# Kernel optimization log

Measured on AMD Instinct MI355X. Metric: run time of the kernel, lower is better.

Reference implementation:

```python
import jax, jax.numpy as jnp
import numpy as np

D_IN = 4097   # 4096 obj feat + 1 depth
D_H1 = 512
D_H2 = 256
N_HEADS = 4
D_HEAD = D_H2 // N_HEADS
D_FF = 512


def setup_inputs() -> dict:
    key = jax.random.key(0)
    ks = jax.random.split(key, 20)
    B, T, N = 2, 100, 30
    s = lambda *sh: 1.0 / np.sqrt(sh[0])
    inp = {
        "object_features": jax.random.normal(ks[0], (B, T, N, 4096), jnp.float32),
        "object_depths": jax.random.uniform(ks[1], (B, T, N, 1), jnp.float32),
        # spatial encoder (2-layer fully-connected message passing)
        "W1a": jax.random.normal(ks[2], (D_IN, D_H1), jnp.float32) * s(D_IN),
        "W2a": jax.random.normal(ks[3], (D_IN, D_H1), jnp.float32) * s(D_IN),
        "b1a": jnp.zeros((D_H1,), jnp.float32),
        "W1b": jax.random.normal(ks[4], (D_H1, D_H2), jnp.float32) * s(D_H1),
        "W2b": jax.random.normal(ks[5], (D_H1, D_H2), jnp.float32) * s(D_H1),
        "b1b": jnp.zeros((D_H2,), jnp.float32),
        # temporal transformer encoder layer (post-LN)
        "Wq": jax.random.normal(ks[6], (D_H2, D_H2), jnp.float32) * s(D_H2),
        "Wk": jax.random.normal(ks[7], (D_H2, D_H2), jnp.float32) * s(D_H2),
        "Wv": jax.random.normal(ks[8], (D_H2, D_H2), jnp.float32) * s(D_H2),
        "Wo": jax.random.normal(ks[9], (D_H2, D_H2), jnp.float32) * s(D_H2),
        "ln1_g": jnp.ones((D_H2,), jnp.float32),
        "ln1_b": jnp.zeros((D_H2,), jnp.float32),
        "Wf1": jax.random.normal(ks[10], (D_H2, D_FF), jnp.float32) * s(D_H2),
        "bf1": jnp.zeros((D_FF,), jnp.float32),
        "Wf2": jax.random.normal(ks[11], (D_FF, D_H2), jnp.float32) * s(D_FF),
        "bf2": jnp.zeros((D_H2,), jnp.float32),
        "ln2_g": jnp.ones((D_H2,), jnp.float32),
        "ln2_b": jnp.zeros((D_H2,), jnp.float32),
        # classifier
        "Wc": jax.random.normal(ks[12], (D_H2, 1), jnp.float32) * s(D_H2),
        "bc": jnp.zeros((1,), jnp.float32),
    }
    return inp


def _layer_norm(x, g, b, eps=1e-5):
    mu = jnp.mean(x, axis=-1, keepdims=True)
    var = jnp.var(x, axis=-1, keepdims=True)
    return (x - mu) * jax.lax.rsqrt(var + eps) * g + b


def _forward(object_features, object_depths, W1a, W2a, b1a, W1b, W2b, b1b,
             Wq, Wk, Wv, Wo, ln1_g, ln1_b, Wf1, bf1, Wf2, bf2, ln2_g, ln2_b,
             Wc, bc):
    B, T, N, _ = object_features.shape
    x = jnp.concatenate([object_features, object_depths], axis=-1)  # (B,T,N,4097)
    # fully-connected graph (torch.combinations, both directions):
    # aggregated message for node i = mean over all j != i.
    def mp(h, Ws, Wn, b):
        neigh = (jnp.sum(h, axis=2, keepdims=True) - h) / (N - 1)
        return jax.nn.relu(h @ Ws + neigh @ Wn + b)
    h = mp(x, W1a, W2a, b1a)      # (B,T,N,512)
    h = mp(h, W1b, W2b, b1b)      # (B,T,N,256)
    g = jnp.mean(h, axis=2)       # global mean pool -> (B,T,256)
    # temporal transformer encoder (self-attention over T, post-LN)
    q = (g @ Wq).reshape(B, T, N_HEADS, D_HEAD)
    k = (g @ Wk).reshape(B, T, N_HEADS, D_HEAD)
    v = (g @ Wv).reshape(B, T, N_HEADS, D_HEAD)
    scores = jnp.einsum("bthd,bshd->bhts", q, k) / np.sqrt(D_HEAD)
    attn = jax.nn.softmax(scores, axis=-1)
    ctx = jnp.einsum("bhts,bshd->bthd", attn, v).reshape(B, T, D_H2) @ Wo
    y = _layer_norm(g + ctx, ln1_g, ln1_b)
    ff = jax.nn.relu(y @ Wf1 + bf1) @ Wf2 + bf2
    z = _layer_norm(y + ff, ln2_g, ln2_b)  # (B,T,256)
    # dropout is identity in eval mode -> probs2 == probs, uncertainty == 0
    logits = (z @ Wc + bc).squeeze(-1)     # (B,T)
    probs = jax.nn.sigmoid(logits)
    uncertainty = jnp.zeros_like(probs)
    return probs, uncertainty


def reference(object_features, object_depths, W1a, W2a, b1a, W1b, W2b, b1b,
              Wq, Wk, Wv, Wo, ln1_g, ln1_b, Wf1, bf1, Wf2, bf2, ln2_g, ln2_b,
              Wc, bc):
    return _forward(object_features, object_depths, W1a, W2a, b1a, W1b, W2b,
                    b1b, Wq, Wk, Wv, Wo, ln1_g, ln1_b, Wf1, bf1, Wf2, bf2,
                    ln2_g, ln2_b, Wc, bc)
```

## Files before the change

kernel.cpp:

```cpp
#include <hip/hip_runtime.h>
#include <hip/hip_bf16.h>
#include <stdint.h>

typedef unsigned short u16;
typedef __attribute__((ext_vector_type(8))) short short8;
typedef __attribute__((ext_vector_type(4))) float floatx4;
typedef __attribute__((ext_vector_type(4))) unsigned short ushort4_t;

#define BT 200
#define NOBJ 30
#define KP2 4224
#define DIN 4097
#define DH1 512
#define DH2 256
#define DFF 512
#define MPAD 6016
#define CHZ 176
#define NBIGW (132*16)
#define NSMALL 512
#define NCONV (BT*3)
#define NZERO 128

__device__ __forceinline__ u16 f2bf(float f) {
    union { float f; uint32_t u; } c; c.f = f;
    uint32_t u = c.u;
    u += 0x7FFF + ((u >> 16) & 1);
    return (u16)(u >> 16);
}

__device__ __forceinline__ void load16_lds(const u16* g, u16* l) {
    __builtin_amdgcn_global_load_lds(
        (const __attribute__((address_space(1))) void*)g,
        (__attribute__((address_space(3))) void*)l, 16, 0, 0);
}

__device__ __forceinline__ size_t tile_off(int ytile, int row, int c8) {
    int z = c8 / CHZ, rem = c8 - z * CHZ;
    int i = rem >> 3, kw = rem & 7;
    int ks = kw ^ (row & 7);
    return ((((size_t)(ytile * 3 + z) * 22 + i) * 128 + row) * 64) + ks * 8;
}

__global__ void prep_all(const float* __restrict__ W1a, const float* __restrict__ W2a,
                         const float* __restrict__ W1b, const float* __restrict__ W2b,
                         const float* __restrict__ feat, const float* __restrict__ depth,
                         u16* __restrict__ Wc1T, u16* __restrict__ W2aTs,
                         u16* __restrict__ Wc2T, u16* __restrict__ W2bTs,
                         u16* __restrict__ XbT, u16* __restrict__ SbT,
                         float* __restrict__ zeroBase, size_t zeroQuads) {
    __shared__ float t1[32][33];
    __shared__ float t2[32][33];
    int bid = blockIdx.x, tid = threadIdx.x;
    if (bid < NCONV) {
        int bt = bid / 3;
        int c8 = (bid % 3) * 256 + tid;
        if (c8 >= 528) return;
        int k8 = c8 * 8;
        int zc = c8 / CHZ, rem = c8 - zc * CHZ;
        int ic = rem >> 3, kwc = rem & 7;
        float s[8] = {};
        if (k8 < 4096) {
            const float* fb = feat + (size_t)bt * NOBJ * 4096 + k8;
            #pragma unroll 1
            for (int n0 = 0; n0 < NOBJ; n0 += 6) {
                float4 va[6], vb[6];
                #pragma unroll
                for (int u = 0; u < 6; u++) {
                    const float* p = fb + (size_t)(n0 + u) * 4096;
                    va[u] = *(const float4*)p;
                    vb[u] = *(const float4*)(p + 4);
                }
                #pragma unroll
                for (int u = 0; u < 6; u++) {
                    int r = bt * NOBJ + n0 + u;
                    float v[8] = {va[u].x, va[u].y, va[u].z, va[u].w,
                                  vb[u].x, vb[u].y, vb[u].z, vb[u].w};
                    short8 o;
                    #pragma unroll
                    for (int e = 0; e < 8; e++) { s[e] += v[e]; o[e] = (short)f2bf(v[e]); }
                    size_t off = ((((size_t)((r >> 7) * 3 + zc) * 22 + ic) * 128
                                   + (r & 127)) * 64) + (size_t)(kwc ^ (r & 7)) * 8;
                    *(short8*)(XbT + off) = o;
                }
            }
        } else {
            for (int n = 0; n < NOBJ; n++) {
                int r = bt * NOBJ + n;
                short8 o = {};
                if (k8 == 4096) {
                    float d = depth[r];
                    s[0] += d;
                    o[0] = (short)f2bf(d);
                }
                size_t off = ((((size_t)((r >> 7) * 3 + zc) * 22 + ic) * 128
                               + (r & 127)) * 64) + (size_t)(kwc ^ (r & 7)) * 8;
                *(short8*)(XbT + off) = o;
            }
        }
        short8 so;
        #pragma unroll
        for (int e = 0; e < 8; e++) so[e] = (short)f2bf(s[e]);
        {
            int r = bt;
            size_t off = ((((size_t)((r >> 7) * 3 + zc) * 22 + ic) * 128
                           + (r & 127)) * 64) + (size_t)(kwc ^ (r & 7)) * 8;
            *(short8*)(SbT + off) = so;
        }
    } else if (bid < NCONV + NZERO) {
        int zid = bid - NCONV;
        float4* p = (float4*)zeroBase;
        float4 zz = {0.f, 0.f, 0.f, 0.f};
        for (size_t idx = (size_t)zid * 256 + tid; idx < zeroQuads; idx += (size_t)NZERO * 256)
            p[idx] = zz;
    } else if (bid < NCONV + NZERO + NSMALL) {
        int idx = (bid - NCONV - NZERO) * 256 + tid;
        int j = idx >> 9, k = idx & 511;
        float a = W1b[k * DH2 + j];
        float b = W2b[k * DH2 + j] * (1.f / 29.f);
        Wc2T[j * DH1 + k]  = f2bf(a - b);
        W2bTs[j * DH1 + k] = f2bf(b);
    } else {
        int b2 = bid - NCONV - NZERO - NSMALL;
        int kb = (b2 % 132) * 32, jb = (b2 / 132) * 32;
        int tx = tid & 31, ty = tid >> 5;
        #pragma unroll
        for (int r = 0; r < 32; r += 8) {
            int k = kb + ty + r, j = jb + tx;
            float a = 0.f, b = 0.f;
            if (k < DIN) { a = W1a[k * DH1 + j]; b = W2a[k * DH1 + j]; }
            float bs = b * (1.f / 29.f);
            t1[ty + r][tx] = a - bs;
            t2[ty + r][tx] = bs;
        }
        __syncthreads();
        #pragma unroll
        for (int r = 0; r < 32; r += 8) {
            int j = jb + ty + r, k = kb + tx;
            int x = j >> 7, row = j & 127;
            size_t off = tile_off(x, row, k >> 3) + (k & 7);
            Wc1T[off]  = f2bf(t1[tx][ty + r]);
            W2aTs[off] = f2bf(t2[tx][ty + r]);
        }
    }
}

__global__ __launch_bounds__(256) void gemmA(
    const u16* __restrict__ XbT, const u16* __restrict__ WaT,
    const u16* __restrict__ SbT, const u16* __restrict__ WsT,
    float* __restrict__ hacc, float* __restrict__ uOut) {
    __shared__ __align__(16) u16 Al[8192];
    __shared__ __align__(16) u16 Bl[8192];
    int bid = blockIdx.x;
    const u16 *Abase, *Bbase;
    float* outF;
    int m0, n0, M;
    if (bid < 564) {
        int x = bid & 3, y = (bid >> 2) % 47, z = bid / 188;
        Abase = XbT + (size_t)((y * 3 + z) * 22) * 8192;
        Bbase = WaT + (size_t)((x * 3 + z) * 22) * 8192;
        outF = hacc; M = 6000; m0 = y * 128; n0 = x * 128;
    } else {
        int rem = bid - 564;
        int x = rem & 3, y = (rem >> 2) & 1, z = rem >> 3;
        Abase = SbT + (size_t)((y * 3 + z) * 22) * 8192;
        Bbase = WsT + (size_t)((x * 3 + z) * 22) * 8192;
        outF = uOut; M = BT; m0 = y * 128; n0 = x * 128;
    }
    int tid = threadIdx.x, lane = tid & 63, w = tid >> 6;
    floatx4 acc[4][4] = {};
    int lrow = lane & 15, q = lane >> 4;
    int wm = (w & 1) * 64, wn = (w >> 1) * 64;
    int swz = lrow & 7;

    for (int i = 0; i < 22; i++) {
        const u16* as = Abase + (size_t)i * 8192;
        const u16* bs = Bbase + (size_t)i * 8192;
        #pragma unroll
        for (int it = 0; it < 4; it++) {
            load16_lds(as + (it * 256 + tid) * 8, Al + it * 2048 + w * 512);
            load16_lds(bs + (it * 256 + tid) * 8, Bl + it * 2048 + w * 512);
        }
        __syncthreads();
        #pragma unroll
        for (int h = 0; h < 2; h++) {
            int ci = h * 4 + q;
            int so = (ci ^ swz) * 8;
            short8 af[4], bfv[4];
            #pragma unroll
            for (int ii = 0; ii < 4; ii++)
                af[ii] = *(short8*)(Al + (wm + ii * 16 + lrow) * 64 + so);
            #pragma unroll
            for (int j = 0; j < 4; j++)
                bfv[j] = *(short8*)(Bl + (wn + j * 16 + lrow) * 64 + so);
            #pragma unroll
            for (int ii = 0; ii < 4; ii++)
                #pragma unroll
                for (int j = 0; j < 4; j++)
                    acc[ii][j] = __builtin_amdgcn_mfma_f32_16x16x32_bf16(af[ii], bfv[j], acc[ii][j], 0, 0, 0);
        }
        __syncthreads();
    }

    #pragma unroll
    for (int ii = 0; ii < 4; ii++)
        #pragma unroll
        for (int j = 0; j < 4; j++)
            #pragma unroll
            for (int r = 0; r < 4; r++) {
                int row = m0 + wm + ii * 16 + q * 4 + r;
                int col = n0 + wn + j * 16 + lrow;
                if (row < M)
                    atomicAdd(&outF[(size_t)row * DH1 + col], acc[ii][j][r]);
            }
}

__global__ __launch_bounds__(256) void gemmB(
    const u16* __restrict__ hb, const u16* __restrict__ Wc2T,
    const u16* __restrict__ Shb, const u16* __restrict__ W2bTs,
    float* __restrict__ hacc2, float* __restrict__ u2Out) {
    __shared__ __align__(16) u16 Al[64 * 64];
    __shared__ __align__(16) u16 Bl[128 * 64];
    int bid = blockIdx.x;
    const u16 *A, *B;
    float* outF;
    int m0, n0, kbeg, M;
    if (bid < 376) {
        int x = bid & 1, y = (bid >> 1) % 94, z = bid / 188;
        A = hb; B = Wc2T; outF = hacc2; M = 6000;
        m0 = y * 64; n0 = x * 128; kbeg = z * 256;
    } else {
        int rem = bid - 376;
        int x = rem & 1, y = (rem >> 1) & 3, z = rem >> 3;
        A = Shb; B = W2bTs; outF = u2Out; M = BT;
        m0 = y * 64; n0 = x * 128; kbeg = z * 256;
    }
    int kend = kbeg + 256;
    const int N = DH2, K = DH1;
    int tid = threadIdx.x;
    int lane = tid & 63, w = tid >> 6;
    int srow = tid >> 3, kslot = tid & 7;
    floatx4 acc[2][4] = {};
    int lrow = lane & 15, q = lane >> 4;
    int wm = (w & 1) * 32, wn = (w >> 1) * 64;
    int swz = lrow & 7;

    for (int kb = kbeg; kb < kend; kb += 64) {
        #pragma unroll
        for (int it = 0; it < 2; it++) {
            int row = it * 32 + srow;
            int kph = kslot ^ (row & 7);
            load16_lds(A + (size_t)(m0 + row) * K + kb + kph * 8,
                       Al + it * 2048 + w * 512);
        }
        #pragma unroll
        for (int it = 0; it < 4; it++) {
            int row = it * 32 + srow;
            int kph = kslot ^ (row & 7);
            load16_lds(B + (size_t)(n0 + row) * K + kb + kph * 8,
                       Bl + it * 2048 + w * 512);
        }
        __syncthreads();
        #pragma unroll
        for (int h = 0; h < 2; h++) {
            int ci = h * 4 + q;
            int so = (ci ^ swz) * 8;
            short8 af[2], bfv[4];
            #pragma unroll
            for (int i = 0; i < 2; i++)
                af[i] = *(short8*)(Al + (wm + i * 16 + lrow) * 64 + so);
            #pragma unroll
            for (int j = 0; j < 4; j++)
                bfv[j] = *(short8*)(Bl + (wn + j * 16 + lrow) * 64 + so);
            #pragma unroll
            for (int i = 0; i < 2; i++)
                #pragma unroll
                for (int j = 0; j < 4; j++)
                    acc[i][j] = __builtin_amdgcn_mfma_f32_16x16x32_bf16(af[i], bfv[j], acc[i][j], 0, 0, 0);
        }
        __syncthreads();
    }

    #pragma unroll
    for (int i = 0; i < 2; i++)
        #pragma unroll
        for (int j = 0; j < 4; j++)
            #pragma unroll
            for (int r = 0; r < 4; r++) {
                int row = m0 + wm + i * 16 + q * 4 + r;
                int col = n0 + wn + j * 16 + lrow;
                if (row < M)
                    atomicAdd(&outF[(size_t)row * N + col], acc[i][j][r]);
            }
}

__global__ void reduce1(const float* __restrict__ hacc, const float* __restrict__ u,
                        const float* __restrict__ b1a,
                        u16* __restrict__ hb, u16* __restrict__ Shb) {
    __shared__ float sl[128];
    int bt = blockIdx.x, c0 = blockIdx.y * 128;
    int lc = threadIdx.x & 127, rp = threadIdx.x >> 7;
    int col = c0 + lc;
    float ub = u[bt * DH1 + col] + b1a[col];
    float s = 0.f;
    for (int n = rp; n < NOBJ; n += 2) {
        float v = hacc[(size_t)(bt * NOBJ + n) * DH1 + col] + ub;
        v = v > 0.f ? v : 0.f;
        hb[(size_t)(bt * NOBJ + n) * DH1 + col] = f2bf(v);
        s += v;
    }
    if (rp == 0) sl[lc] = s;
    __syncthreads();
    if (rp == 1) Shb[bt * DH1 + col] = f2bf(sl[lc] + s);
}

__global__ void reduce2_qkv(const float* __restrict__ hacc2, const float* __restrict__ u2,
                            const float* __restrict__ b1b,
                            const float* __restrict__ Wq, const float* __restrict__ Wk,
                            const float* __restrict__ Wv,
                            float* __restrict__ g, float* __restrict__ q,
                            float* __restrict__ k, float* __restrict__ v) {
    __shared__ float gl[DH2];
    int bt = blockIdx.x, j = threadIdx.x;
    float ub = u2[bt * DH2 + j] + b1b[j];
    float a = 0.f;
    for (int n = 0; n < NOBJ; n++) {
        float vv = hacc2[(size_t)(bt * NOBJ + n) * DH2 + j] + ub;
        a += vv > 0.f ? vv : 0.f;
    }
    a *= (1.f / 30.f);
    gl[j] = a;
    g[bt * DH2 + j] = a;
    __syncthreads();
    float aq = 0.f, ak = 0.f, av = 0.f;
    for (int kk = 0; kk < DH2; kk++) {
        float x = gl[kk];
        aq += x * Wq[kk * DH2 + j];
        ak += x * Wk[kk * DH2 + j];
        av += x * Wv[kk * DH2 + j];
    }
    q[bt * DH2 + j] = aq;
    k[bt * DH2 + j] = ak;
    v[bt * DH2 + j] = av;
}

__device__ __forceinline__ float block_sum256(float v, volatile float* red) {
    #pragma unroll
    for (int o = 32; o > 0; o >>= 1) v += __shfl_down(v, o);
    int w = threadIdx.x >> 6;
    __syncthreads();
    if ((threadIdx.x & 63) == 0) red[w] = v;
    __syncthreads();
    return red[0] + red[1] + red[2] + red[3];
}

__global__ void attn_head(const float* __restrict__ qg, const float* __restrict__ kg,
                          const float* __restrict__ vg, const float* __restrict__ g,
                          const float* __restrict__ Wo,
                          const float* __restrict__ ln1g, const float* __restrict__ ln1b,
                          const float* __restrict__ Wf1, const float* __restrict__ bf1,
                          const float* __restrict__ Wf2, const float* __restrict__ bf2,
                          const float* __restrict__ ln2g, const float* __restrict__ ln2b,
                          const float* __restrict__ Wc, const float* __restrict__ bc,
                          float* __restrict__ out) {
    __shared__ float ql[DH2];
    __shared__ float scl[4][128];
    __shared__ float ctxl[DH2];
    __shared__ float yl[DH2];
    __shared__ float ffl[DFF];
    __shared__ float red[4];
    int row = blockIdx.x, tid = threadIdx.x;
    int base = (row >= 100) ? 100 : 0;
    ql[tid] = qg[row * DH2 + tid];
    __syncthreads();

    for (int p = tid; p < 512; p += 256) {
        int h = p >> 7, s = p & 127;
        if (s < 100) {
            const float* kr = kg + (size_t)(base + s) * DH2 + h * 64;
            float a = 0.f;
            #pragma unroll 8
            for (int d = 0; d < 64; d++) a += ql[h * 64 + d] * kr[d];
            scl[h][s] = a * 0.125f;
        }
    }
    __syncthreads();

    {
        int w = tid >> 6, lane = tid & 63;
        int s2 = 64 + lane;
        float a  = scl[w][lane];
        float b2 = (s2 < 100) ? scl[w][s2] : -1e30f;
        float m = fmaxf(a, b2);
        #pragma unroll
        for (int o = 32; o > 0; o >>= 1) m = fmaxf(m, __shfl_down(m, o));
        m = __shfl(m, 0);
        float e1 = __expf(a - m);
        float e2 = (s2 < 100) ? __expf(b2 - m) : 0.f;
        float sm = e1 + e2;
        #pragma unroll
        for (int o = 32; o > 0; o >>= 1) sm += __shfl_down(sm, o);
        sm = __shfl(sm, 0);
        float r = 1.f / sm;
        scl[w][lane] = e1 * r;
        if (s2 < 100) scl[w][s2] = e2 * r;
    }
    __syncthreads();

    {
        int h = tid >> 6;
        float o = 0.f;
        for (int s = 0; s < 100; s++)
            o += scl[h][s] * vg[(size_t)(base + s) * DH2 + tid];
        ctxl[tid] = o;
    }
    __syncthreads();

    float o = 0.f;
    for (int kk = 0; kk < DH2; kk++) o += ctxl[kk] * Wo[kk * DH2 + tid];
    float t = g[row * DH2 + tid] + o;
    float mu  = block_sum256(t, red) * (1.f / DH2);
    float ex2 = block_sum256(t * t, red) * (1.f / DH2);
    float y = (t - mu) * rsqrtf(ex2 - mu * mu + 1e-5f) * ln1g[tid] + ln1b[tid];
    yl[tid] = y;
    __syncthreads();
    for (int jj = tid; jj < DFF; jj += 256) {
        float a = bf1[jj];
        for (int kk = 0; kk < DH2; kk++) a += yl[kk] * Wf1[kk * DFF + jj];
        ffl[jj] = a > 0.f ? a : 0.f;
    }
    __syncthreads();
    float o2 = bf2[tid];
    for (int kk = 0; kk < DFF; kk++) o2 += ffl[kk] * Wf2[kk * DH2 + tid];
    float z0 = y + o2;
    float mu2  = block_sum256(z0, red) * (1.f / DH2);
    float ex22 = block_sum256(z0 * z0, red) * (1.f / DH2);
    float z = (z0 - mu2) * rsqrtf(ex22 - mu2 * mu2 + 1e-5f) * ln2g[tid] + ln2b[tid];
    float logit = block_sum256(z * Wc[tid], red) + bc[0];
    if (tid == 0) {
        out[row]      = 1.f / (1.f + __expf(-logit));
        out[BT + row] = 0.f;
    }
}

extern "C" void kernel_launch(void* const* d_in, const int* in_sizes, int n_in,
                              void* d_out, int out_size, void* d_ws, size_t ws_size,
                              hipStream_t stream) {
    const float* feat  = (const float*)d_in[0];
    const float* depth = (const float*)d_in[1];
    const float* W1a = (const float*)d_in[2];
    const float* W2a = (const float*)d_in[3];
    const float* b1a = (const float*)d_in[4];
    const float* W1b = (const float*)d_in[5];
    const float* W2b = (const float*)d_in[6];
    const float* b1b = (const float*)d_in[7];
    const float* Wq  = (const float*)d_in[8];
    const float* Wk  = (const float*)d_in[9];
    const float* Wv  = (const float*)d_in[10];
    const float* Wo  = (const float*)d_in[11];
    const float* ln1g = (const float*)d_in[12];
    const float* ln1b = (const float*)d_in[13];
    const float* Wf1 = (const float*)d_in[14];
    const float* bf1 = (const float*)d_in[15];
    const float* Wf2 = (const float*)d_in[16];
    const float* bf2 = (const float*)d_in[17];
    const float* ln2g = (const float*)d_in[18];
    const float* ln2b = (const float*)d_in[19];
    const float* Wc  = (const float*)d_in[20];
    const float* bc  = (const float*)d_in[21];
    float* out = (float*)d_out;
    char* ws = (char*)d_ws;

    size_t off = 0;
    u16* XbT   = (u16*)(ws + off); off += (size_t)MPAD * KP2 * 2;
    u16* SbT   = (u16*)(ws + off); off += (size_t)256 * KP2 * 2;
    u16* Wc1T  = (u16*)(ws + off); off += (size_t)DH1 * KP2 * 2;
    u16* W2aTs = (u16*)(ws + off); off += (size_t)DH1 * KP2 * 2;
    u16* Wc2T  = (u16*)(ws + off); off += (size_t)DH2 * DH1 * 2;
    u16* W2bTs = (u16*)(ws + off); off += (size_t)DH2 * DH1 * 2;
    u16* Shb   = (u16*)(ws + off); off += (size_t)256 * DH1 * 2;
    char* zBase = ws + off;
    float* hacc  = (float*)(ws + off); off += (size_t)6000 * DH1 * 4;
    float* hacc2 = (float*)(ws + off); off += (size_t)6000 * DH2 * 4;
    float* u     = (float*)(ws + off); off += (size_t)BT * DH1 * 4;
    float* u2    = (float*)(ws + off); off += (size_t)BT * DH2 * 4;
    size_t zeroQuads = (size_t)(ws + off - zBase) / 16;
    u16* hb = XbT;
    float* g = (float*)SbT;
    float* q = g + BT * DH2;
    float* k = q + BT * DH2;
    float* v = k + BT * DH2;

    prep_all<<<NBIGW + NSMALL + NCONV + NZERO, 256, 0, stream>>>(
        W1a, W2a, W1b, W2b, feat, depth,
        Wc1T, W2aTs, Wc2T, W2bTs, XbT, SbT, (float*)zBase, zeroQuads);
    gemmA<<<564 + 24, 256, 0, stream>>>(XbT, Wc1T, SbT, W2aTs, hacc, u);
    reduce1<<<dim3(BT, 4), 256, 0, stream>>>(hacc, u, b1a, hb, Shb);
    gemmB<<<376 + 16, 256, 0, stream>>>(hb, Wc2T, Shb, W2bTs, hacc2, u2);
    reduce2_qkv<<<BT, DH2, 0, stream>>>(hacc2, u2, b1b, Wq, Wk, Wv, g, q, k, v);
    attn_head<<<BT, DH2, 0, stream>>>(q, k, v, g, Wo, ln1g, ln1b, Wf1, bf1,
                                      Wf2, bf2, ln2g, ln2b, Wc, bc, out);
}
```

Baseline: 375.9 us.

## Double-buffer LDS tiles in gemmA/gemmB and remap blocks across XCDs

Both GEMM kernels now use two LDS buffers: the next K-tile is loaded asynchronously into the other buffer while MFMAs run on the current one, with explicit waitcnt and barriers replacing __syncthreads. Block IDs in the main GEMM paths are also remapped so that consecutive logical tiles land on the same XCD, improving L2 locality for shared A/B panels. This doubles LDS use per block, which may lower occupancy, and relies on hand-placed scheduling barriers for correctness.

```diff
diff --git a/kernel.cpp b/kernel.cpp
--- a/kernel.cpp
+++ b/kernel.cpp
@@ -148,14 +148,16 @@
     const u16* __restrict__ XbT, const u16* __restrict__ WaT,
     const u16* __restrict__ SbT, const u16* __restrict__ WsT,
     float* __restrict__ hacc, float* __restrict__ uOut) {
-    __shared__ __align__(16) u16 Al[8192];
-    __shared__ __align__(16) u16 Bl[8192];
+    __shared__ __align__(16) u16 Al[2][8192];
+    __shared__ __align__(16) u16 Bl[2][8192];
     int bid = blockIdx.x;
     const u16 *Abase, *Bbase;
     float* outF;
     int m0, n0, M;
     if (bid < 564) {
-        int x = bid & 3, y = (bid >> 2) % 47, z = bid / 188;
+        int xcd = bid & 7, slot = bid >> 3;
+        int lid = (xcd < 4 ? xcd * 71 : 284 + (xcd - 4) * 70) + slot;
+        int x = lid & 3, y = (lid >> 2) % 47, z = lid / 188;
         Abase = XbT + (size_t)((y * 3 + z) * 22) * 8192;
         Bbase = WaT + (size_t)((x * 3 + z) * 22) * 8192;
         outF = hacc; M = 6000; m0 = y * 128; n0 = x * 128;
@@ -172,15 +174,30 @@
     int wm = (w & 1) * 64, wn = (w >> 1) * 64;
     int swz = lrow & 7;
 
+    #pragma unroll
+    for (int it = 0; it < 4; it++) {
+        load16_lds(Abase + (it * 256 + tid) * 8, &Al[0][it * 2048 + w * 512]);
+        load16_lds(Bbase + (it * 256 + tid) * 8, &Bl[0][it * 2048 + w * 512]);
+    }
+    asm volatile("s_waitcnt vmcnt(0)" ::: "memory");
+    __builtin_amdgcn_s_barrier();
+    __builtin_amdgcn_sched_barrier(0);
+
+    int cur = 0;
     for (int i = 0; i < 22; i++) {
-        const u16* as = Abase + (size_t)i * 8192;
-        const u16* bs = Bbase + (size_t)i * 8192;
-        #pragma unroll
-        for (int it = 0; it < 4; it++) {
-            load16_lds(as + (it * 256 + tid) * 8, Al + it * 2048 + w * 512);
-            load16_lds(bs + (it * 256 + tid) * 8, Bl + it * 2048 + w * 512);
-        }
-        __syncthreads();
+        if (i + 1 < 22) {
+            const u16* as = Abase + (size_t)(i + 1) * 8192;
+            const u16* bs = Bbase + (size_t)(i + 1) * 8192;
+            int nxt = cur ^ 1;
+            #pragma unroll
+            for (int it = 0; it < 4; it++) {
+                load16_lds(as + (it * 256 + tid) * 8, &Al[nxt][it * 2048 + w * 512]);
+                load16_lds(bs + (it * 256 + tid) * 8, &Bl[nxt][it * 2048 + w * 512]);
+            }
+        }
+        __builtin_amdgcn_sched_barrier(0);
+        const u16* Ac = &Al[cur][0];
+        const u16* Bc = &Bl[cur][0];
         #pragma unroll
         for (int h = 0; h < 2; h++) {
             int ci = h * 4 + q;
@@ -188,17 +205,21 @@
             short8 af[4], bfv[4];
             #pragma unroll
             for (int ii = 0; ii < 4; ii++)
-                af[ii] = *(short8*)(Al + (wm + ii * 16 + lrow) * 64 + so);
+                af[ii] = *(short8*)(Ac + (wm + ii * 16 + lrow) * 64 + so);
             #pragma unroll
             for (int j = 0; j < 4; j++)
-                bfv[j] = *(short8*)(Bl + (wn + j * 16 + lrow) * 64 + so);
+                bfv[j] = *(short8*)(Bc + (wn + j * 16 + lrow) * 64 + so);
             #pragma unroll
             for (int ii = 0; ii < 4; ii++)
                 #pragma unroll
                 for (int j = 0; j < 4; j++)
                     acc[ii][j] = __builtin_amdgcn_mfma_f32_16x16x32_bf16(af[ii], bfv[j], acc[ii][j], 0, 0, 0);
         }
-        __syncthreads();
+        __builtin_amdgcn_sched_barrier(0);
+        asm volatile("s_waitcnt vmcnt(0) lgkmcnt(0)" ::: "memory");
+        __builtin_amdgcn_s_barrier();
+        __builtin_amdgcn_sched_barrier(0);
+        cur ^= 1;
     }
 
     #pragma unroll
@@ -218,14 +239,16 @@
     const u16* __restrict__ hb, const u16* __restrict__ Wc2T,
     const u16* __restrict__ Shb, const u16* __restrict__ W2bTs,
     float* __restrict__ hacc2, float* __restrict__ u2Out) {
-    __shared__ __align__(16) u16 Al[64 * 64];
-    __shared__ __align__(16) u16 Bl[128 * 64];
+    __shared__ __align__(16) u16 Al[2][4096];
+    __shared__ __align__(16) u16 Bl[2][8192];
     int bid = blockIdx.x;
     const u16 *A, *B;
     float* outF;
     int m0, n0, kbeg, M;
     if (bid < 376) {
-        int x = bid & 1, y = (bid >> 1) % 94, z = bid / 188;
+        int xcd = bid & 7, slot = bid >> 3;
+        int lid = xcd * 47 + slot;
+        int x = lid & 1, y = (lid >> 1) % 94, z = lid / 188;
         A = hb; B = Wc2T; outF = hacc2; M = 6000;
         m0 = y * 64; n0 = x * 128; kbeg = z * 256;
     } else {
@@ -234,7 +257,6 @@
         A = Shb; B = W2bTs; outF = u2Out; M = BT;
         m0 = y * 64; n0 = x * 128; kbeg = z * 256;
     }
-    int kend = kbeg + 256;
     const int N = DH2, K = DH1;
     int tid = threadIdx.x;
     int lane = tid & 63, w = tid >> 6;
@@ -244,22 +266,34 @@
     int wm = (w & 1) * 32, wn = (w >> 1) * 64;
     int swz = lrow & 7;
 
-    for (int kb = kbeg; kb < kend; kb += 64) {
+    auto stage = [&](int buf, int kb) {
         #pragma unroll
         for (int it = 0; it < 2; it++) {
             int row = it * 32 + srow;
             int kph = kslot ^ (row & 7);
             load16_lds(A + (size_t)(m0 + row) * K + kb + kph * 8,
-                       Al + it * 2048 + w * 512);
+                       &Al[buf][it * 2048 + w * 512]);
         }
         #pragma unroll
         for (int it = 0; it < 4; it++) {
             int row = it * 32 + srow;
             int kph = kslot ^ (row & 7);
             load16_lds(B + (size_t)(n0 + row) * K + kb + kph * 8,
-                       Bl + it * 2048 + w * 512);
-        }
-        __syncthreads();
+                       &Bl[buf][it * 2048 + w * 512]);
+        }
+    };
+
+    stage(0, kbeg);
+    asm volatile("s_waitcnt vmcnt(0)" ::: "memory");
+    __builtin_amdgcn_s_barrier();
+    __builtin_amdgcn_sched_barrier(0);
+
+    int cur = 0;
+    for (int t = 0; t < 4; t++) {
+        if (t + 1 < 4) stage(cur ^ 1, kbeg + (t + 1) * 64);
+        __builtin_amdgcn_sched_barrier(0);
+        const u16* Ac = &Al[cur][0];
+        const u16* Bc = &Bl[cur][0];
         #pragma unroll
         for (int h = 0; h < 2; h++) {
             int ci = h * 4 + q;
@@ -267,17 +301,21 @@
             short8 af[2], bfv[4];
             #pragma unroll
             for (int i = 0; i < 2; i++)
-                af[i] = *(short8*)(Al + (wm + i * 16 + lrow) * 64 + so);
+                af[i] = *(short8*)(Ac + (wm + i * 16 + lrow) * 64 + so);
             #pragma unroll
             for (int j = 0; j < 4; j++)
-                bfv[j] = *(short8*)(Bl + (wn + j * 16 + lrow) * 64 + so);
+                bfv[j] = *(short8*)(Bc + (wn + j * 16 + lrow) * 64 + so);
             #pragma unroll
             for (int i = 0; i < 2; i++)
                 #pragma unroll
                 for (int j = 0; j < 4; j++)
                     acc[i][j] = __builtin_amdgcn_mfma_f32_16x16x32_bf16(af[i], bfv[j], acc[i][j], 0, 0, 0);
         }
-        __syncthreads();
+        __builtin_amdgcn_sched_barrier(0);
+        asm volatile("s_waitcnt vmcnt(0) lgkmcnt(0)" ::: "memory");
+        __builtin_amdgcn_s_barrier();
+        __builtin_amdgcn_sched_barrier(0);
+        cur ^= 1;
     }
 
     #pragma unroll
```

Result: slower. 394.0 us (+4.8%).
